# Performance work log

Hardware: AMD Instinct MI355X
Metric: run time of the kernel (lower is better)

Reference implementation:

```python
import jax, jax.numpy as jnp
import numpy as np

EMBED_DIM = 1024
NUM_HEADS = 16
HEAD_DIM = EMBED_DIM // NUM_HEADS
N, S = 4, 2048


def setup_inputs() -> dict:
    key = jax.random.key(0)
    ks = jax.random.split(key, 11)
    s = 1.0 / np.sqrt(EMBED_DIM)
    inp = {
        'query': jax.random.normal(ks[0], (N, S, EMBED_DIM), jnp.float32),
        'key': jax.random.normal(ks[1], (N, S, EMBED_DIM), jnp.float32),
        'value': jax.random.normal(ks[2], (N, S, EMBED_DIM), jnp.float32),
        'wq': jax.random.normal(ks[3], (EMBED_DIM, EMBED_DIM), jnp.float32) * s,
        'bq': jnp.zeros((EMBED_DIM,), jnp.float32),
        'wk': jax.random.normal(ks[4], (EMBED_DIM, EMBED_DIM), jnp.float32) * s,
        'bk': jnp.zeros((EMBED_DIM,), jnp.float32),
        'wv': jax.random.normal(ks[5], (EMBED_DIM, EMBED_DIM), jnp.float32) * s,
        'bv': jnp.zeros((EMBED_DIM,), jnp.float32),
        'wo': jax.random.normal(ks[6], (EMBED_DIM, EMBED_DIM), jnp.float32) * s,
        'bo': jnp.zeros((EMBED_DIM,), jnp.float32),
    }
    return inp


def reference(query, key, value, wq, bq, wk, bk, wv, bv, wo, bo):
    n = query.shape[0]
    # projections: y = x @ W^T + b (torch nn.Linear convention)
    Q = query @ wq.T + bq
    K = key @ wk.T + bk
    V = value @ wv.T + bv
    # [n, h, s, d]
    Q = Q.reshape(n, -1, NUM_HEADS, HEAD_DIM).transpose(0, 2, 1, 3)
    K = K.reshape(n, -1, NUM_HEADS, HEAD_DIM).transpose(0, 2, 1, 3)
    V = V.reshape(n, -1, NUM_HEADS, HEAD_DIM).transpose(0, 2, 1, 3)
    energy = jnp.einsum('nhqd,nhkd->nhqk', Q, K)
    attn = jax.nn.softmax(energy / jnp.sqrt(jnp.float32(HEAD_DIM)), axis=-1)
    out = jnp.einsum('nhqk,nhkd->nhqd', attn, V)
    out = out.transpose(0, 2, 1, 3).reshape(n, -1, NUM_HEADS * HEAD_DIM)
    return out @ wo.T + bo
```

## Files before the change

kernel.cpp:

```cpp
#include <hip/hip_runtime.h>
#include <hip/hip_bf16.h>

#define EMBED 1024
#define SEQ   2048
#define NB    4
#define NH    16
#define HD    64
#define MROWS (NB*SEQ)
#define WELEM (EMBED*EMBED)

typedef __attribute__((ext_vector_type(4))) float  f32x4;
typedef __attribute__((ext_vector_type(8))) short  s16x8;

#define MFMA16(a,b,c) __builtin_amdgcn_mfma_f32_16x16x32_bf16((a),(b),(c),0,0,0)

__device__ __forceinline__ unsigned short f2bf(float f) {
    union { float f; unsigned int u; } v; v.f = f;
    unsigned int r = v.u + 0x7fffu + ((v.u >> 16) & 1u);
    return (unsigned short)(r >> 16);
}
__device__ __forceinline__ unsigned int cvtpk(float a, float b) {
    unsigned int r;
    asm("v_cvt_pk_bf16_f32 %0, %1, %2" : "=v"(r) : "v"(a), "v"(b));
    return r;
}
__device__ __forceinline__ float exp2r(float x) {
    float r;
    asm("v_exp_f32 %0, %1" : "=v"(r) : "v"(x));
    return r;
}
__device__ __forceinline__ void gload16(const void* g, void* l) {
    __builtin_amdgcn_global_load_lds(
        (const __attribute__((address_space(1))) void*)g,
        (__attribute__((address_space(3))) void*)l, 16, 0, 0);
}

#define SC2 0.18033688f

__global__ __launch_bounds__(256) void conv_w(
    const float* __restrict__ wq, const float* __restrict__ wk,
    const float* __restrict__ wv, const float* __restrict__ wo,
    unsigned short* __restrict__ Wbf)
{
    const int i   = blockIdx.x*256 + threadIdx.x;
    const int seg = i >> 17;
    const int off = i & 131071;
    const float* src = seg == 0 ? wq : (seg == 1 ? wk : (seg == 2 ? wv : wo));
    const float sc   = seg == 0 ? SC2 : 1.f;
    const float4 a = *(const float4*)(src + (size_t)off*8);
    const float4 b = *(const float4*)(src + (size_t)off*8 + 4);
    uint4 o;
    o.x = cvtpk(a.x*sc, a.y*sc); o.y = cvtpk(a.z*sc, a.w*sc);
    o.z = cvtpk(b.x*sc, b.y*sc); o.w = cvtpk(b.z*sc, b.w*sc);
    *(uint4*)(Wbf + (size_t)seg*WELEM + (size_t)off*8) = o;
}

template<int WMODE>
__global__ __launch_bounds__(256) void qkv_fused(
    const float* __restrict__ Aq, const float* __restrict__ Ak,
    const float* __restrict__ Av,
    const float* __restrict__ wq, const float* __restrict__ wk,
    const float* __restrict__ wv, const unsigned short* __restrict__ Wbf,
    const float* __restrict__ bq, const float* __restrict__ bk,
    const float* __restrict__ bv,
    unsigned short* __restrict__ Qp, unsigned short* __restrict__ Kp,
    unsigned short* __restrict__ Vt)
{
    __shared__ unsigned short Ald[128*72];
    __shared__ unsigned short Bld[WMODE ? 128*64 : 128*72];
    const int t   = threadIdx.x;
    const int bm  = blockIdx.x, bn = blockIdx.y;
    const int sel = bn >> 3, bnl = bn & 7;
    const float* Af   = sel == 0 ? Aq : (sel == 1 ? Ak : Av);
    const float* Wf   = sel == 0 ? wq : (sel == 1 ? wk : wv);
    const unsigned short* Wb = Wbf + (size_t)sel*WELEM;
    const float* bias = sel == 0 ? bq : (sel == 1 ? bk : bv);

    const int wid = t >> 6, lane = t & 63, l15 = lane & 15, blk = lane >> 4;
    const int wr  = wid >> 1, wc = wid & 1;

    f32x4 acc[4][4] = {};

    for (int kt = 0; kt < EMBED/64; ++kt) {
        if (WMODE == 1) {
            #pragma unroll
            for (int j = 0; j < 4; ++j) {
                const int u = j*256 + t, row = u >> 3, slot = u & 7;
                const unsigned short* src = Wb + (size_t)(bnl*128+row)*EMBED
                                               + kt*64 + (slot ^ (row & 7))*8;
                gload16(src, (char*)Bld + j*4096 + wid*1024);
            }
        }
        #pragma unroll
        for (int j = 0; j < 8; ++j) {
            int f = t + 256*j, row = f >> 4, c4 = f & 15;
            float4 v = *(const float4*)(Af + (size_t)(bm*128+row)*EMBED + kt*64 + c4*4);
            *(uint2*)&Ald[row*72 + c4*4] = make_uint2(cvtpk(v.x,v.y), cvtpk(v.z,v.w));
        }
        if (WMODE == 0) {
            #pragma unroll
            for (int j = 0; j < 8; ++j) {
                int f = t + 256*j, row = f >> 4, c4 = f & 15;
                float4 v = *(const float4*)(Wf + (size_t)(bnl*128+row)*EMBED + kt*64 + c4*4);
                *(uint2*)&Bld[row*72 + c4*4] = make_uint2(cvtpk(v.x,v.y), cvtpk(v.z,v.w));
            }
        } else {
            asm volatile("s_waitcnt vmcnt(0)" ::: "memory");
        }
        __syncthreads();
        #pragma unroll
        for (int ks = 0; ks < 2; ++ks) {
            s16x8 af[4], bf[4];
            #pragma unroll
            for (int mt = 0; mt < 4; ++mt)
                af[mt] = *(const s16x8*)&Ald[(wr*64 + mt*16 + l15)*72 + ks*32 + blk*8];
            #pragma unroll
            for (int nt = 0; nt < 4; ++nt) {
                const int rb = wc*64 + nt*16 + l15;
                if (WMODE == 1)
                    bf[nt] = *(const s16x8*)((const char*)Bld + rb*128
                                 + ((ks*64 + blk*16) ^ ((rb & 7) << 4)));
                else
                    bf[nt] = *(const s16x8*)&Bld[rb*72 + ks*32 + blk*8];
            }
            #pragma unroll
            for (int mt = 0; mt < 4; ++mt)
                #pragma unroll
                for (int nt = 0; nt < 4; ++nt)
                    acc[mt][nt] = MFMA16(af[mt], bf[nt], acc[mt][nt]);
        }
        __syncthreads();
    }

    const float scale = (sel == 0) ? SC2 : 1.0f;
    float bv4[4];
    #pragma unroll
    for (int nt = 0; nt < 4; ++nt) {
        float bb = bias[bnl*128 + wc*64 + nt*16 + l15];
        bv4[nt] = (WMODE == 1) ? bb*scale : bb;
    }

    #pragma unroll
    for (int mt = 0; mt < 4; ++mt) {
        #pragma unroll
        for (int nt = 0; nt < 4; ++nt) {
            const int m0 = bm*128 + wr*64 + mt*16 + blk*4;
            const int n  = bnl*128 + wc*64 + nt*16 + l15;
            f32x4 a = acc[mt][nt];
            if (sel < 2) {
                unsigned short* Yb = (sel == 0) ? Qp : Kp;
                #pragma unroll
                for (int r = 0; r < 4; ++r) {
                    float val = (WMODE == 1) ? (a[r] + bv4[nt])
                                             : (a[r] + bv4[nt]) * scale;
                    Yb[(size_t)(m0+r)*EMBED + n] = f2bf(val);
                }
            } else {
                const int b = m0 >> 11, s = m0 & (SEQ-1);
                const int h = n >> 6,  d = n & (HD-1);
                ushort4 pk;
                pk.x = f2bf(a[0] + bv4[nt]); pk.y = f2bf(a[1] + bv4[nt]);
                pk.z = f2bf(a[2] + bv4[nt]); pk.w = f2bf(a[3] + bv4[nt]);
                *(ushort4*)&Vt[(((size_t)b*NH + h)*HD + d)*SEQ + s] = pk;
            }
        }
    }
}

template<int WMODE>
__global__ __launch_bounds__(256) void gemm_out(
    const unsigned short* __restrict__ Ab, const float* __restrict__ W,
    const unsigned short* __restrict__ Wb,
    const float* __restrict__ bias, float* __restrict__ Yf)
{
    __shared__ unsigned short Ald[128*64];
    __shared__ unsigned short Bld[WMODE ? 128*64 : 128*72];
    const int t   = threadIdx.x;
    const int bm  = blockIdx.x, bn = blockIdx.y;
    const int wid = t >> 6, lane = t & 63, l15 = lane & 15, blk = lane >> 4;
    const int wr  = wid >> 1, wc = wid & 1;

    f32x4 acc[4][4] = {};

    for (int kt = 0; kt < EMBED/64; ++kt) {
        #pragma unroll
        for (int j = 0; j < 4; ++j) {
            const int u = j*256 + t, row = u >> 3, slot = u & 7;
            const unsigned short* src = Ab + (size_t)(bm*128+row)*EMBED
                                           + kt*64 + (slot ^ (row & 7))*8;
            gload16(src, (char*)Ald + j*4096 + wid*1024);
        }
        if (WMODE == 1) {
            #pragma unroll
            for (int j = 0; j < 4; ++j) {
                const int u = j*256 + t, row = u >> 3, slot = u & 7;
                const unsigned short* src = Wb + (size_t)(bn*128+row)*EMBED
                                               + kt*64 + (slot ^ (row & 7))*8;
                gload16(src, (char*)Bld + j*4096 + wid*1024);
            }
        } else {
            #pragma unroll
            for (int j = 0; j < 8; ++j) {
                int f = t + 256*j, row = f >> 4, c4 = f & 15;
                float4 v = *(const float4*)(W + (size_t)(bn*128+row)*EMBED + kt*64 + c4*4);
                *(uint2*)&Bld[row*72 + c4*4] = make_uint2(cvtpk(v.x,v.y), cvtpk(v.z,v.w));
            }
        }
        asm volatile("s_waitcnt vmcnt(0)" ::: "memory");
        __syncthreads();
        #pragma unroll
        for (int ks = 0; ks < 2; ++ks) {
            s16x8 af[4], bf[4];
            #pragma unroll
            for (int mt = 0; mt < 4; ++mt) {
                const int ra = wr*64 + mt*16 + l15;
                af[mt] = *(const s16x8*)((const char*)Ald + ra*128
                             + ((ks*64 + blk*16) ^ ((ra & 7) << 4)));
            }
            #pragma unroll
            for (int nt = 0; nt < 4; ++nt) {
                const int rb = wc*64 + nt*16 + l15;
                if (WMODE == 1)
                    bf[nt] = *(const s16x8*)((const char*)Bld + rb*128
                                 + ((ks*64 + blk*16) ^ ((rb & 7) << 4)));
                else
                    bf[nt] = *(const s16x8*)&Bld[rb*72 + ks*32 + blk*8];
            }
            #pragma unroll
            for (int mt = 0; mt < 4; ++mt)
                #pragma unroll
                for (int nt = 0; nt < 4; ++nt)
                    acc[mt][nt] = MFMA16(af[mt], bf[nt], acc[mt][nt]);
        }
        __syncthreads();
    }

    float bv4[4];
    #pragma unroll
    for (int nt = 0; nt < 4; ++nt)
        bv4[nt] = bias[bn*128 + wc*64 + nt*16 + l15];

    #pragma unroll
    for (int mt = 0; mt < 4; ++mt)
        #pragma unroll
        for (int nt = 0; nt < 4; ++nt) {
            const int m0 = bm*128 + wr*64 + mt*16 + blk*4;
            const int n  = bn*128 + wc*64 + nt*16 + l15;
            f32x4 a = acc[mt][nt];
            #pragma unroll
            for (int r = 0; r < 4; ++r)
                Yf[(size_t)(m0+r)*EMBED + n] = a[r] + bv4[nt];
        }
}

__global__ __launch_bounds__(512) void attn_fwd(
    const unsigned short* __restrict__ Qp,
    const unsigned short* __restrict__ Kp,
    const unsigned short* __restrict__ Vt,
    unsigned short* __restrict__ ctx)
{
    __shared__ unsigned short Kld[2][64*64];
    __shared__ unsigned short Vld[2][64*64];
    __shared__ unsigned short Pld[8][32*64];

    const int t = threadIdx.x, wid = t >> 6, lane = t & 63;
    const int l15 = lane & 15, blk = lane >> 4;
    const int bh = blockIdx.x, qb = blockIdx.y;
    const int b = bh >> 4, h = bh & (NH-1);
    const int q0 = qb*256 + wid*32;

    s16x8 qf[2][2];
    #pragma unroll
    for (int qs = 0; qs < 2; ++qs) {
        const unsigned short* qp = Qp + (size_t)(b*SEQ + q0 + qs*16 + l15)*EMBED + h*HD;
        qf[qs][0] = *(const s16x8*)(qp + blk*8);
        qf[qs][1] = *(const s16x8*)(qp + 32 + blk*8);
    }

    const unsigned short* kb = Kp + (size_t)b*SEQ*EMBED + h*HD;
    const unsigned short* vb = Vt + (size_t)bh*HD*SEQ;

    const int u  = wid*64 + lane;
    const int r0 = u >> 3;
    const int s0 = ((((u&7)<<4) ^ ((r0&7)<<4)) >> 1);
    const unsigned short* kS = kb + (size_t)r0*EMBED + s0;
    const unsigned short* vS = vb + (size_t)r0*SEQ  + s0;

    unsigned short* pl = &Pld[wid][0];
    const int rc0 = (blk*16) ^ ((l15 & 7) << 4);
    const int rc1 = rc0 ^ 64;

    s16x8 onesf;
    #pragma unroll
    for (int j = 0; j < 8; ++j) onesf[j] = (short)0x3F80;

    f32x4 o[2][4] = {};
    f32x4 sacc[2] = {};

    gload16(kS, (char*)Kld[0] + wid*1024);
    gload16(vS, (char*)Vld[0] + wid*1024);
    asm volatile("s_waitcnt vmcnt(0)" ::: "memory");
    __syncthreads();

    int cur = 0;
    for (int tt = 0; tt < SEQ/64; ++tt) {
        if (tt + 1 < SEQ/64) {
            const size_t ko = (size_t)(tt+1)*64;
            gload16(kS + ko*EMBED, (char*)Kld[cur^1] + wid*1024);
            gload16(vS + ko,       (char*)Vld[cur^1] + wid*1024);
        }

        const char* kbase = (const char*)Kld[cur];
        const char* vbase = (const char*)Vld[cur];

        f32x4 sc[2][4];
        #pragma unroll
        for (int qs = 0; qs < 2; ++qs)
            #pragma unroll
            for (int kt = 0; kt < 4; ++kt)
                sc[qs][kt] = f32x4{0.f,0.f,0.f,0.f};
        __builtin_amdgcn_s_setprio(1);
        #pragma unroll
        for (int kt = 0; kt < 4; ++kt) {
            const char* krow = kbase + (kt*16 + l15)*128;
            s16x8 ka0 = *(const s16x8*)(krow + rc0);
            s16x8 ka1 = *(const s16x8*)(krow + rc1);
            #pragma unroll
            for (int qs = 0; qs < 2; ++qs) {
                sc[qs][kt] = MFMA16(ka0, qf[qs][0], sc[qs][kt]);
                sc[qs][kt] = MFMA16(ka1, qf[qs][1], sc[qs][kt]);
            }
        }
        __builtin_amdgcn_s_setprio(0);

        #pragma unroll
        for (int qs = 0; qs < 2; ++qs) {
            #pragma unroll
            for (int kt = 0; kt < 4; ++kt) {
                const float e0 = exp2r(sc[qs][kt][0]);
                const float e1 = exp2r(sc[qs][kt][1]);
                const float e2 = exp2r(sc[qs][kt][2]);
                const float e3 = exp2r(sc[qs][kt][3]);
                const int off = (qs*16 + l15)*128 + ((kt*32 + blk*8) ^ ((l15 & 7) << 4));
                *(uint2*)((char*)pl + off) = make_uint2(cvtpk(e0,e1), cvtpk(e2,e3));
            }
        }

        s16x8 pa[2][2];
        #pragma unroll
        for (int qs = 0; qs < 2; ++qs) {
            const char* prow = (const char*)pl + (qs*16 + l15)*128;
            pa[qs][0] = *(const s16x8*)(prow + rc0);
            pa[qs][1] = *(const s16x8*)(prow + rc1);
        }
        __builtin_amdgcn_s_setprio(1);
        #pragma unroll
        for (int qs = 0; qs < 2; ++qs) {
            sacc[qs] = MFMA16(pa[qs][0], onesf, sacc[qs]);
            sacc[qs] = MFMA16(pa[qs][1], onesf, sacc[qs]);
        }
        #pragma unroll
        for (int dt = 0; dt < 4; ++dt) {
            const char* vrow = vbase + (dt*16 + l15)*128;
            s16x8 vb0 = *(const s16x8*)(vrow + rc0);
            s16x8 vb1 = *(const s16x8*)(vrow + rc1);
            #pragma unroll
            for (int qs = 0; qs < 2; ++qs) {
                o[qs][dt] = MFMA16(pa[qs][0], vb0, o[qs][dt]);
                o[qs][dt] = MFMA16(pa[qs][1], vb1, o[qs][dt]);
            }
        }
        __builtin_amdgcn_s_setprio(0);

        asm volatile("s_waitcnt vmcnt(0)" ::: "memory");
        __syncthreads();
        cur ^= 1;
    }

    #pragma unroll
    for (int qs = 0; qs < 2; ++qs) {
        float li[4];
        #pragma unroll
        for (int r = 0; r < 4; ++r) li[r] = 1.f / sacc[qs][r];
        unsigned short* cp = ctx + (size_t)(b*SEQ + q0 + qs*16)*EMBED + h*HD;
        #pragma unroll
        for (int dt = 0; dt < 4; ++dt)
            #pragma unroll
            for (int r = 0; r < 4; ++r)
                cp[(size_t)(blk*4 + r)*EMBED + dt*16 + l15] = f2bf(o[qs][dt][r] * li[r]);
    }
}

extern "C" void kernel_launch(void* const* d_in, const int* in_sizes, int n_in,
                              void* d_out, int out_size, void* d_ws, size_t ws_size,
                              hipStream_t stream)
{
    const float* q  = (const float*)d_in[0];
    const float* k  = (const float*)d_in[1];
    const float* v  = (const float*)d_in[2];
    const float* wq = (const float*)d_in[3];
    const float* bq = (const float*)d_in[4];
    const float* wk = (const float*)d_in[5];
    const float* bk = (const float*)d_in[6];
    const float* wv = (const float*)d_in[7];
    const float* bv = (const float*)d_in[8];
    const float* wo = (const float*)d_in[9];
    const float* bo = (const float*)d_in[10];

    unsigned short* Qp  = (unsigned short*)d_out;
    unsigned short* Kp  = Qp + (size_t)MROWS*EMBED;
    unsigned short* Vt  = (unsigned short*)d_ws;
    unsigned short* ctx = Vt + (size_t)MROWS*EMBED;
    unsigned short* Wbf = ctx + (size_t)MROWS*EMBED;
    float* out = (float*)d_out;

    const bool pre = ws_size >= (size_t)40*1024*1024;

    dim3 tpb(256);
    if (pre) {
        conv_w<<<2048, tpb, 0, stream>>>(wq, wk, wv, wo, Wbf);
        qkv_fused<1><<<dim3(MROWS/128, 24), tpb, 0, stream>>>(
            q, k, v, wq, wk, wv, Wbf, bq, bk, bv, Qp, Kp, Vt);
    } else {
        qkv_fused<0><<<dim3(MROWS/128, 24), tpb, 0, stream>>>(
            q, k, v, wq, wk, wv, Wbf, bq, bk, bv, Qp, Kp, Vt);
    }
    attn_fwd<<<dim3(NB*NH, SEQ/256), dim3(512), 0, stream>>>(Qp, Kp, Vt, ctx);
    if (pre) {
        gemm_out<1><<<dim3(MROWS/128, EMBED/128), tpb, 0, stream>>>(
            ctx, wo, Wbf + (size_t)3*WELEM, bo, out);
    } else {
        gemm_out<0><<<dim3(MROWS/128, EMBED/128), tpb, 0, stream>>>(
            ctx, wo, Wbf, bo, out);
    }
}
```

Before: 182.4 us.

## Triple-buffer bf16 weight tiles with async global-to-LDS prefetch in QKV GEMM

```diff
diff --git a/kernel.cpp b/kernel.cpp
--- a/kernel.cpp
+++ b/kernel.cpp
@@ -67,7 +67,7 @@
     unsigned short* __restrict__ Vt)
 {
     __shared__ unsigned short Ald[128*72];
-    __shared__ unsigned short Bld[WMODE ? 128*64 : 128*72];
+    __shared__ unsigned short Bld[WMODE ? 3*128*64 : 128*72];
     const int t   = threadIdx.x;
     const int bm  = blockIdx.x, bn = blockIdx.y;
     const int sel = bn >> 3, bnl = bn & 7;
@@ -81,55 +81,102 @@
 
     f32x4 acc[4][4] = {};
 
-    for (int kt = 0; kt < EMBED/64; ++kt) {
-        if (WMODE == 1) {
-            #pragma unroll
-            for (int j = 0; j < 4; ++j) {
-                const int u = j*256 + t, row = u >> 3, slot = u & 7;
-                const unsigned short* src = Wb + (size_t)(bnl*128+row)*EMBED
-                                               + kt*64 + (slot ^ (row & 7))*8;
-                gload16(src, (char*)Bld + j*4096 + wid*1024);
-            }
-        }
-        #pragma unroll
-        for (int j = 0; j < 8; ++j) {
-            int f = t + 256*j, row = f >> 4, c4 = f & 15;
-            float4 v = *(const float4*)(Af + (size_t)(bm*128+row)*EMBED + kt*64 + c4*4);
-            *(uint2*)&Ald[row*72 + c4*4] = make_uint2(cvtpk(v.x,v.y), cvtpk(v.z,v.w));
-        }
-        if (WMODE == 0) {
+    if (WMODE == 1) {
+        const int u_   = 0;
+        (void)u_;
+        #pragma unroll
+        for (int j = 0; j < 4; ++j) {
+            const int u = j*256 + t, row = u >> 3, slot = u & 7;
+            gload16(Wb + (size_t)(bnl*128+row)*EMBED + 0*64 + (slot ^ (row & 7))*8,
+                    (char*)Bld + 0*16384 + j*4096 + wid*1024);
+        }
+        #pragma unroll
+        for (int j = 0; j < 4; ++j) {
+            const int u = j*256 + t, row = u >> 3, slot = u & 7;
+            gload16(Wb + (size_t)(bnl*128+row)*EMBED + 1*64 + (slot ^ (row & 7))*8,
+                    (char*)Bld + 1*16384 + j*4096 + wid*1024);
+        }
+        asm volatile("s_waitcnt vmcnt(4)" ::: "memory");
+        __builtin_amdgcn_sched_barrier(0);
+        __builtin_amdgcn_s_barrier();
+
+        for (int kt = 0; kt < 16; ++kt) {
+            if (kt + 2 < 16) {
+                const int bsel = (kt + 2) % 3;
+                #pragma unroll
+                for (int j = 0; j < 4; ++j) {
+                    const int u = j*256 + t, row = u >> 3, slot = u & 7;
+                    gload16(Wb + (size_t)(bnl*128+row)*EMBED + (kt+2)*64
+                               + (slot ^ (row & 7))*8,
+                            (char*)Bld + bsel*16384 + j*4096 + wid*1024);
+                }
+            }
+            #pragma unroll
+            for (int j = 0; j < 8; ++j) {
+                int f = t + 256*j, row = f >> 4, c4 = f & 15;
+                float4 v = *(const float4*)(Af + (size_t)(bm*128+row)*EMBED + kt*64 + c4*4);
+                *(uint2*)&Ald[row*72 + c4*4] = make_uint2(cvtpk(v.x,v.y), cvtpk(v.z,v.w));
+            }
+            asm volatile("s_waitcnt lgkmcnt(0)" ::: "memory");
+            __builtin_amdgcn_sched_barrier(0);
+            __builtin_amdgcn_s_barrier();
+
+            const char* Bbase = (const char*)Bld + (kt % 3)*16384;
+            #pragma unroll
+            for (int ks = 0; ks < 2; ++ks) {
+                s16x8 af[4], bf[4];
+                #pragma unroll
+                for (int mt = 0; mt < 4; ++mt)
+                    af[mt] = *(const s16x8*)&Ald[(wr*64 + mt*16 + l15)*72 + ks*32 + blk*8];
+                #pragma unroll
+                for (int nt = 0; nt < 4; ++nt) {
+                    const int rb = wc*64 + nt*16 + l15;
+                    bf[nt] = *(const s16x8*)(Bbase + rb*128
+                                 + ((ks*64 + blk*16) ^ ((rb & 7) << 4)));
+                }
+                #pragma unroll
+                for (int mt = 0; mt < 4; ++mt)
+                    #pragma unroll
+                    for (int nt = 0; nt < 4; ++nt)
+                        acc[mt][nt] = MFMA16(af[mt], bf[nt], acc[mt][nt]);
+            }
+            if (kt < 14) { asm volatile("s_waitcnt vmcnt(4) lgkmcnt(0)" ::: "memory"); }
+            else         { asm volatile("s_waitcnt vmcnt(0) lgkmcnt(0)" ::: "memory"); }
+            __builtin_amdgcn_sched_barrier(0);
+            __builtin_amdgcn_s_barrier();
+        }
+    } else {
+        for (int kt = 0; kt < 16; ++kt) {
+            #pragma unroll
+            for (int j = 0; j < 8; ++j) {
+                int f = t + 256*j, row = f >> 4, c4 = f & 15;
+                float4 v = *(const float4*)(Af + (size_t)(bm*128+row)*EMBED + kt*64 + c4*4);
+                *(uint2*)&Ald[row*72 + c4*4] = make_uint2(cvtpk(v.x,v.y), cvtpk(v.z,v.w));
+            }
             #pragma unroll
             for (int j = 0; j < 8; ++j) {
                 int f = t + 256*j, row = f >> 4, c4 = f & 15;
                 float4 v = *(const float4*)(Wf + (size_t)(bnl*128+row)*EMBED + kt*64 + c4*4);
                 *(uint2*)&Bld[row*72 + c4*4] = make_uint2(cvtpk(v.x,v.y), cvtpk(v.z,v.w));
             }
-        } else {
-            asm volatile("s_waitcnt vmcnt(0)" ::: "memory");
-        }
-        __syncthreads();
-        #pragma unroll
-        for (int ks = 0; ks < 2; ++ks) {
-            s16x8 af[4], bf[4];
-            #pragma unroll
-            for (int mt = 0; mt < 4; ++mt)
-                af[mt] = *(const s16x8*)&Ald[(wr*64 + mt*16 + l15)*72 + ks*32 + blk*8];
-            #pragma unroll
-            for (int nt = 0; nt < 4; ++nt) {
-                const int rb = wc*64 + nt*16 + l15;
-                if (WMODE == 1)
-                    bf[nt] = *(const s16x8*)((const char*)Bld + rb*128
-                                 + ((ks*64 + blk*16) ^ ((rb & 7) << 4)));
-                else
-                    bf[nt] = *(const s16x8*)&Bld[rb*72 + ks*32 + blk*8];
-            }
-            #pragma unroll
-            for (int mt = 0; mt < 4; ++mt)
+            __syncthreads();
+            #pragma unroll
+            for (int ks = 0; ks < 2; ++ks) {
+                s16x8 af[4], bf[4];
+                #pragma unroll
+                for (int mt = 0; mt < 4; ++mt)
+                    af[mt] = *(const s16x8*)&Ald[(wr*64 + mt*16 + l15)*72 + ks*32 + blk*8];
                 #pragma unroll
                 for (int nt = 0; nt < 4; ++nt)
-                    acc[mt][nt] = MFMA16(af[mt], bf[nt], acc[mt][nt]);
-        }
-        __syncthreads();
+                    bf[nt] = *(const s16x8*)&Bld[(wc*64 + nt*16 + l15)*72 + ks*32 + blk*8];
+                #pragma unroll
+                for (int mt = 0; mt < 4; ++mt)
+                    #pragma unroll
+                    for (int nt = 0; nt < 4; ++nt)
+                        acc[mt][nt] = MFMA16(af[mt], bf[nt], acc[mt][nt]);
+            }
+            __syncthreads();
+        }
     }
 
     const float scale = (sel == 0) ? SC2 : 1.0f;
```

After: 201.3 us. 1.1x slower.
